# Performance work log

Measured on AMD Instinct MI355X. Metric: run time of the kernel, lower is better.

## Reference

```python
import jax, jax.numpy as jnp
import numpy as np

B, L, D_MODEL, D_FF, H = 2, 2048, 512, 512, 8
DK = D_FF // H


def _lin(key, fan_in, fan_out):
    k1, k2 = jax.random.split(key)
    lim = 1.0 / np.sqrt(fan_in)
    W = jax.random.uniform(k1, (fan_in, fan_out), jnp.float32, -lim, lim)
    b = jax.random.uniform(k2, (fan_out,), jnp.float32, -lim, lim)
    return W, b


def setup_inputs() -> dict:
    key = jax.random.key(0)
    ks = jax.random.split(key, 13)
    x = jax.random.normal(ks[0], (B, L, D_MODEL), jnp.float32)
    x_knowledge = jax.random.normal(ks[1], (B, L, D_MODEL), jnp.float32)
    Wv, bv = _lin(ks[2], D_MODEL, D_FF)
    Wk, bk = _lin(ks[3], D_MODEL, D_FF)
    Wq, bq = _lin(ks[4], D_MODEL, D_FF)
    Wkf, bkf = _lin(ks[5], D_MODEL, D_FF)
    Wqf, bqf = _lin(ks[6], D_MODEL, D_FF)
    Wq2, bq2 = _lin(ks[7], D_FF, D_FF)
    Wk2, bk2 = _lin(ks[8], D_FF, D_FF)
    Wkf2, bkf2 = _lin(ks[9], D_FF, D_FF)
    Wqf2, bqf2 = _lin(ks[10], D_FF, D_FF)
    Wo, bo = _lin(ks[11], D_FF, D_MODEL)
    return dict(x=x, x_knowledge=x_knowledge, Wv=Wv, bv=bv, Wk=Wk, bk=bk,
                Wq=Wq, bq=bq, Wkf=Wkf, bkf=bkf, Wqf=Wqf, bqf=bqf,
                Wq2=Wq2, bq2=bq2, Wk2=Wk2, bk2=bk2, Wqf2=Wqf2, bqf2=bqf2,
                Wkf2=Wkf2, bkf2=bkf2, Wo=Wo, bo=bo)


def reference(x, x_knowledge, Wv, bv, Wk, bk, Wq, bq, Wkf, bkf, Wqf, bqf,
              Wq2, bq2, Wk2, bk2, Wqf2, bqf2, Wkf2, bkf2, Wo, bo):
    b, l, _ = x.shape
    # first projections from d_model -> d_ff
    v = x @ Wv + bv
    k = x @ Wk + bk
    q = x @ Wq + bq
    k_fei = x_knowledge @ Wkf + bkf
    q_fei = x_knowledge @ Wqf + bqf
    # second projections + NONSTANDARD head split: raw reshape (B,L,d_ff)->(B,h,L,dk)
    q = (q @ Wq2 + bq2).reshape(b, H, l, DK)
    k = (k @ Wk2 + bk2).reshape(b, H, l, DK)
    q_fei = (q_fei @ Wqf2 + bqf2).reshape(b, H, l, DK)
    k_fei = (k_fei @ Wkf2 + bkf2).reshape(b, H, l, DK)
    scale = 1.0 / np.sqrt(2.0 * DK).astype(np.float32)
    att = jnp.einsum('bhld,bhmd->bhlm', q, k) * scale
    att_fei = jnp.einsum('bhld,bhmd->bhlm', q_fei, k_fei) * scale
    score = jax.nn.softmax(att + att_fei, axis=-1)  # dropout is identity at eval
    v = v.reshape(b, H, l, DK)
    out = jnp.einsum('bhlm,bhmd->bhld', score, v).reshape(b, l, D_FF)
    return out @ Wo + bo
```

## Files before the change

### kernel.cpp

```cpp
#include <hip/hip_runtime.h>
#include <hip/hip_bf16.h>

typedef unsigned short u16;
typedef unsigned int   u32;
typedef __attribute__((ext_vector_type(8))) short bf16x8;
typedef __attribute__((ext_vector_type(4))) float f32x4;

#define SCALE 0.08838834764831845f
#define SCLOG 0.12752040542575836f

__device__ inline u16 f2bf(float f) {
  u32 u = __builtin_bit_cast(u32, f);
  u = (u + 0x7FFFu + ((u >> 16) & 1u)) >> 16;
  return (u16)u;
}
__device__ inline float bf2f(u16 b) {
  u32 u = (u32)b << 16;
  return __builtin_bit_cast(float, u);
}
__device__ __forceinline__ u16 cvbf(float f) {
  return __builtin_bit_cast(u16, __float2bfloat16(f));
}
__device__ __forceinline__ u32 pkbf(float a, float b) {
  return (u32)cvbf(a) | ((u32)cvbf(b) << 16);
}
__device__ __forceinline__ float fexp2(float x) {
#if __has_builtin(__builtin_amdgcn_exp2f)
  return __builtin_amdgcn_exp2f(x);
#else
  float r; asm("v_exp_f32 %0, %1" : "=v"(r) : "v"(x)); return r;
#endif
}

__device__ __forceinline__ void glds16(const u16* g, u16* l) {
  __builtin_amdgcn_global_load_lds(
      (__attribute__((address_space(1))) void*)g,
      (__attribute__((address_space(3))) void*)l, 16, 0, 0);
}

struct CvPtrs { const float* in[6]; u16* out[6]; int nblk[6]; };

__global__ __launch_bounds__(256) void cvtAll(CvPtrs cp) {
  const int y = blockIdx.y;
  if ((int)blockIdx.x >= cp.nblk[y]) return;
  const float* in = cp.in[y];
  u16* out = cp.out[y];
  const int i = (blockIdx.x * 256 + threadIdx.x) * 8;
  float4 f0 = *(const float4*)(in + i);
  float4 f1 = *(const float4*)(in + i + 4);
  alignas(16) u16 t[8] = {f2bf(f0.x), f2bf(f0.y), f2bf(f0.z), f2bf(f0.w),
                          f2bf(f1.x), f2bf(f1.y), f2bf(f1.z), f2bf(f1.w)};
  *(uint4*)(out + i) = *(const uint4*)t;
}

struct WPtrs { const float* w[10]; const float* b[10]; };

__global__ __launch_bounds__(256) void transposeW(WPtrs p, u16* __restrict__ out,
                                                  float* __restrict__ biasP) {
  __shared__ u16 ts[64][65];
  const int z = blockIdx.z;
  const float sc = (z == 5 || z == 7) ? SCLOG : 1.0f;
  const float* in = p.w[z];
  u16* o = out + (size_t)z * 262144;
  const int t = threadIdx.x;
  const int k0 = blockIdx.y * 64, n0 = blockIdx.x * 64;
  if (blockIdx.x == 0 && blockIdx.y == 0 && (z == 0 || z == 9)) {
    biasP[z * 512 + t]       = p.b[z][t];
    biasP[z * 512 + t + 256] = p.b[z][t + 256];
  }
  for (int pp = 0; pp < 16; ++pp) {
    int id = t + 256 * pp; int r = id >> 6, c = id & 63;
    ts[r][c] = f2bf(in[(size_t)(k0 + r) * 512 + n0 + c] * sc);
  }
  __syncthreads();
  for (int pp = 0; pp < 16; ++pp) {
    int id = t + 256 * pp; int r = id >> 6, c = id & 63;
    o[(size_t)(n0 + r) * 512 + k0 + c] = ts[c][r];
  }
}

struct BEPtrs { const float* b1[4]; const float* w2[4]; const float* b2[4]; };

__global__ __launch_bounds__(256) void biasEff(BEPtrs be, float* __restrict__ biasP) {
  __shared__ float red[16][17];
  const int z = blockIdx.x;
  const int n0 = blockIdx.y * 16;
  const float sc = (z == 0 || z == 2) ? SCLOG : 1.0f;
  const int nl = threadIdx.x & 15, jg = threadIdx.x >> 4;
  const float* b1 = be.b1[z];
  const float* w2 = be.w2[z];
  float s = 0.0f;
  #pragma unroll 4
  for (int jj = 0; jj < 32; ++jj) {
    const int j = jg * 32 + jj;
    s += b1[j] * w2[(size_t)j * 512 + n0 + nl];
  }
  red[jg][nl] = s;
  __syncthreads();
  if (threadIdx.x < 16) {
    float t = 0.0f;
    #pragma unroll
    for (int g = 0; g < 16; ++g) t += red[g][threadIdx.x];
    biasP[(1 + z) * 512 + n0 + threadIdx.x] =
        (t + be.b2[z][n0 + threadIdx.x]) * sc;
  }
}

struct GemmBatch {
  const u16* A[4];
  const u16* Ax;
  int xsplit;
  void* out[5];
  int wrow0, zstride;
};

template <typename TOUT, bool NB>
__global__ __launch_bounds__(256, 4) void gemm4(GemmBatch gb,
    const u16* __restrict__ Wt, const float* __restrict__ biasP) {
  const int tx = blockIdx.x, z = blockIdx.z;
  const u16* A = (tx < gb.xsplit) ? gb.A[z] : gb.Ax;
  const int wrow = gb.wrow0 + z * gb.zstride + tx * 128;
  const int m0 = blockIdx.y * 128;
  const u16* B = Wt + (size_t)wrow * 512;
  const float* bias = biasP + wrow;

  const int t = threadIdx.x, wid = t >> 6, lane = t & 63;
  const int lg = lane >> 4, ln = lane & 15;
  const int wr = wid >> 1, wc = wid & 1;

  __shared__ u16 As[128][64];
  __shared__ u16 Bs[128][64];

  const u16* Ag = A + (size_t)m0 * 512;
  const int lrow = lane >> 3, lch = lane & 7;

  f32x4 acc[4][4];
  #pragma unroll
  for (int i = 0; i < 4; ++i)
    #pragma unroll
    for (int j = 0; j < 4; ++j)
      #pragma unroll
      for (int r = 0; r < 4; ++r) acc[i][j][r] = 0.0f;

  for (int kt = 0; kt < 8; ++kt) {
    #pragma unroll
    for (int c = 0; c < 4; ++c) {
      const int row = (wid * 4 + c) * 8 + lrow;
      const size_t go = (size_t)row * 512 + kt * 64 + lch * 8;
      glds16(Ag + go, &As[(wid * 4 + c) * 8][0]);
      glds16(B  + go, &Bs[(wid * 4 + c) * 8][0]);
    }
    __syncthreads();

    #pragma unroll
    for (int ck = 0; ck < 2; ++ck) {
      bf16x8 af[4], bfr[4];
      #pragma unroll
      for (int mi = 0; mi < 4; ++mi)
        af[mi] = *(const bf16x8*)&As[wr * 64 + mi * 16 + ln][ck * 32 + lg * 8];
      #pragma unroll
      for (int ni = 0; ni < 4; ++ni)
        bfr[ni] = *(const bf16x8*)&Bs[wc * 64 + ni * 16 + ln][ck * 32 + lg * 8];
      #pragma unroll
      for (int mi = 0; mi < 4; ++mi)
        #pragma unroll
        for (int ni = 0; ni < 4; ++ni)
          acc[mi][ni] = __builtin_amdgcn_mfma_f32_16x16x32_bf16(
              af[mi], bfr[ni], acc[mi][ni], 0, 0, 0);
    }
    if (kt < 7) __syncthreads();
  }

  TOUT* C = (TOUT*)gb.out[(wrow >> 9) - (gb.wrow0 >> 9)];
  const int nbase = wrow & 511;
  #pragma unroll
  for (int ni = 0; ni < 4; ++ni) {
    const int colw = wc * 64 + ni * 16 + ln;
    const float bv = NB ? 0.0f : bias[colw];
    const int col = nbase + colw;
    #pragma unroll
    for (int mi = 0; mi < 4; ++mi)
      #pragma unroll
      for (int r = 0; r < 4; ++r) {
        const int row = m0 + wr * 64 + mi * 16 + 4 * lg + r;
        const float val = acc[mi][ni][r] + bv;
        if constexpr (sizeof(TOUT) == 4) C[(size_t)row * 512 + col] = val;
        else                             C[(size_t)row * 512 + col] = f2bf(val);
      }
  }
}

__global__ __launch_bounds__(256) void transposeV(const u16* __restrict__ v1,
                                                  u16* __restrict__ vt) {
  __shared__ u16 ts[64][65];
  const size_t base = (size_t)blockIdx.y * 131072;
  const u16* in = v1 + base;
  u16* out = vt + base;
  const int l0 = blockIdx.x * 64;
  const int t = threadIdx.x;
  const int r = t >> 3, c8 = (t & 7) * 8;
  for (int pp = 0; pp < 2; ++pp) {
    int rr = r + pp * 32;
    *(uint4*)&ts[rr][c8] = *(const uint4*)&in[(size_t)(l0 + rr) * 64 + c8];
  }
  __syncthreads();
  for (int pp = 0; pp < 2; ++pp) {
    int d = r + pp * 32;
    alignas(16) u16 tmp[8];
    #pragma unroll
    for (int i = 0; i < 8; ++i) tmp[i] = ts[c8 + i][d];
    *(uint4*)&out[(size_t)d * 2048 + l0 + c8] = *(const uint4*)tmp;
  }
}

__global__ __launch_bounds__(512) void attn8(
    const u16* __restrict__ q2, const u16* __restrict__ k2,
    const u16* __restrict__ qf2, const u16* __restrict__ kf2,
    const u16* __restrict__ vtg, u16* __restrict__ opart,
    float2* __restrict__ mlbuf) {
  const int id = blockIdx.x;
  const int nid = (id & 7) * 32 + (id >> 3);
  const int split = nid & 1;
  const int qt = (nid >> 1) & 7;
  const int bh = nid >> 4;
  const size_t base = (size_t)bh * 131072;
  const int kv0 = split * 1024;

  const u16* Q  = q2  + base;
  const u16* Qf = qf2 + base;
  u16* Op = opart + (size_t)split * 2097152 + base;

  const int t = threadIdx.x, wid = t >> 6, lane = t & 63;
  const int lg = lane >> 4, ln = lane & 15;
  const int r0 = qt * 256 + wid * 32;

  __shared__ u16 K_s [2][64][64];
  __shared__ u16 Kf_s[2][64][64];
  __shared__ u16 Vt_s[2][64][64];

  const int srow = t >> 3, sch = t & 7;
  const int fsr = (srow & 3) | (((srow >> 3) & 1) << 2);
  const int sw = (sch ^ fsr) * 8;
  const u16* Ksrc  = k2  + base + (size_t)(kv0 + srow) * 64 + sch * 8;
  const u16* Kfsrc = kf2 + base + (size_t)(kv0 + srow) * 64 + sch * 8;
  const u16* Vsrc  = vtg + base + (size_t)srow * 2048 + kv0 + sch * 8;

  bf16x8 aq[2][4];
  #pragma unroll
  for (int qb = 0; qb < 2; ++qb) {
    const int row = r0 + qb * 16 + ln;
    aq[qb][0] = *(const bf16x8*)&Q [row * 64 +      lg * 8];
    aq[qb][1] = *(const bf16x8*)&Q [row * 64 + 32 + lg * 8];
    aq[qb][2] = *(const bf16x8*)&Qf[row * 64 +      lg * 8];
    aq[qb][3] = *(const bf16x8*)&Qf[row * 64 + 32 + lg * 8];
  }

  f32x4 oacc[2][4];
  #pragma unroll
  for (int qb = 0; qb < 2; ++qb)
    #pragma unroll
    for (int df = 0; df < 4; ++df)
      #pragma unroll
      for (int r = 0; r < 4; ++r) oacc[qb][df][r] = 0.0f;
  float m_run[2], l_par[2];
  #pragma unroll
  for (int qb = 0; qb < 2; ++qb) { m_run[qb] = -1e30f; l_par[qb] = 0.0f; }

  const int rbase = 8 * (ln >> 2) + (ln & 3);

  uint4 rk = *(const uint4*)(Ksrc);
  uint4 rf = *(const uint4*)(Kfsrc);
  uint4 rv = *(const uint4*)(Vsrc);
  *(uint4*)&K_s [0][srow][sw] = rk;
  *(uint4*)&Kf_s[0][srow][sw] = rf;
  *(uint4*)&Vt_s[0][srow][sw] = rv;
  __syncthreads();

  int cur = 0;
  for (int kt = 0; kt < 16; ++kt) {
    if (kt < 15) {
      const int ko = (kt + 1) * 4096;
      rk = *(const uint4*)(Ksrc  + ko);
      rf = *(const uint4*)(Kfsrc + ko);
      rv = *(const uint4*)(Vsrc  + (kt + 1) * 64);
    }

    f32x4 s[2][4];
    #pragma unroll
    for (int m = 0; m < 4; ++m) {
      const int rowg = rbase + 4 * (m & 1) + 32 * (m >> 1);
      const int fz = (rowg & 3) | (((rowg >> 3) & 1) << 2);
      bf16x8 a0 = *(const bf16x8*)&K_s [cur][rowg][((0 + lg) ^ fz) * 8];
      bf16x8 a1 = *(const bf16x8*)&K_s [cur][rowg][((4 + lg) ^ fz) * 8];
      bf16x8 a2 = *(const bf16x8*)&Kf_s[cur][rowg][((0 + lg) ^ fz) * 8];
      bf16x8 a3 = *(const bf16x8*)&Kf_s[cur][rowg][((4 + lg) ^ fz) * 8];
      #pragma unroll
      for (int qb = 0; qb < 2; ++qb) {
        f32x4 a;
        #pragma unroll
        for (int r = 0; r < 4; ++r) a[r] = 0.0f;
        a = __builtin_amdgcn_mfma_f32_16x16x32_bf16(a0, aq[qb][0], a, 0, 0, 0);
        a = __builtin_amdgcn_mfma_f32_16x16x32_bf16(a1, aq[qb][1], a, 0, 0, 0);
        a = __builtin_amdgcn_mfma_f32_16x16x32_bf16(a2, aq[qb][2], a, 0, 0, 0);
        a = __builtin_amdgcn_mfma_f32_16x16x32_bf16(a3, aq[qb][3], a, 0, 0, 0);
        s[qb][m] = a;
      }
    }

    float smax[2];
    bool viol = false;
    #pragma unroll
    for (int qb = 0; qb < 2; ++qb) {
      float v = fmaxf(fmaxf(s[qb][0][0], s[qb][0][1]),
                      fmaxf(s[qb][0][2], s[qb][0][3]));
      #pragma unroll
      for (int m = 1; m < 4; ++m)
        v = fmaxf(v, fmaxf(fmaxf(s[qb][m][0], s[qb][m][1]),
                           fmaxf(s[qb][m][2], s[qb][m][3])));
      smax[qb] = v;
      viol = viol || (v > m_run[qb] + 11.0f);
    }
    if (__any(viol)) {
      float corrq[2];
      #pragma unroll
      for (int qb = 0; qb < 2; ++qb) {
        float v = smax[qb];
        v = fmaxf(v, __shfl_xor(v, 16, 64));
        v = fmaxf(v, __shfl_xor(v, 32, 64));
        const float mnew = fmaxf(m_run[qb], v);
        corrq[qb] = fexp2(m_run[qb] - mnew);
        m_run[qb] = mnew;
        l_par[qb] *= corrq[qb];
      }
      #pragma unroll
      for (int qb = 0; qb < 2; ++qb)
        #pragma unroll
        for (int r = 0; r < 4; ++r) {
          const float c = __shfl(corrq[qb], 4 * lg + r, 64);
          #pragma unroll
          for (int df = 0; df < 4; ++df) oacc[qb][df][r] *= c;
        }
    }

    bf16x8 pa[2][2];
    #pragma unroll
    for (int qb = 0; qb < 2; ++qb) {
      float pf[4][4];
      #pragma unroll
      for (int m = 0; m < 4; ++m)
        #pragma unroll
        for (int r = 0; r < 4; ++r) {
          const float p = fexp2(s[qb][m][r] - m_run[qb]);
          l_par[qb] += p;
          pf[m][r] = p;
        }
      #pragma unroll
      for (int kc = 0; kc < 2; ++kc) {
        union { u32 w[4]; bf16x8 v; } U;
        U.w[0] = pkbf(pf[2 * kc][0],     pf[2 * kc][1]);
        U.w[1] = pkbf(pf[2 * kc][2],     pf[2 * kc][3]);
        U.w[2] = pkbf(pf[2 * kc + 1][0], pf[2 * kc + 1][1]);
        U.w[3] = pkbf(pf[2 * kc + 1][2], pf[2 * kc + 1][3]);
        pa[qb][kc] = U.v;
      }
    }

    #pragma unroll
    for (int kc = 0; kc < 2; ++kc)
      #pragma unroll
      for (int df = 0; df < 4; ++df) {
        const int rv = 16 * df + ln;
        const int fz = (rv & 3) | (((rv >> 3) & 1) << 2);
        bf16x8 bv = *(const bf16x8*)&Vt_s[cur][rv][((kc * 4 + lg) ^ fz) * 8];
        oacc[0][df] = __builtin_amdgcn_mfma_f32_16x16x32_bf16(pa[0][kc], bv, oacc[0][df], 0, 0, 0);
        oacc[1][df] = __builtin_amdgcn_mfma_f32_16x16x32_bf16(pa[1][kc], bv, oacc[1][df], 0, 0, 0);
      }

    if (kt < 15) {
      *(uint4*)&K_s [cur ^ 1][srow][sw] = rk;
      *(uint4*)&Kf_s[cur ^ 1][srow][sw] = rf;
      *(uint4*)&Vt_s[cur ^ 1][srow][sw] = rv;
      __syncthreads();
      cur ^= 1;
    }
  }

  #pragma unroll
  for (int qb = 0; qb < 2; ++qb) {
    l_par[qb] += __shfl_xor(l_par[qb], 16, 64);
    l_par[qb] += __shfl_xor(l_par[qb], 32, 64);
  }

  #pragma unroll
  for (int qb = 0; qb < 2; ++qb)
    #pragma unroll
    for (int df = 0; df < 4; ++df)
      #pragma unroll
      for (int r = 0; r < 4; ++r) {
        const int row = r0 + qb * 16 + 4 * lg + r;
        const int col = df * 16 + ln;
        Op[(size_t)row * 64 + col] = f2bf(oacc[qb][df][r]);
      }
  if (lane < 16) {
    #pragma unroll
    for (int qb = 0; qb < 2; ++qb) {
      const int grow = bh * 2048 + r0 + qb * 16 + ln;
      mlbuf[split * 32768 + grow] = make_float2(m_run[qb], l_par[qb]);
    }
  }
}

__global__ __launch_bounds__(256) void combine(
    const u16* __restrict__ opart, const float2* __restrict__ mlbuf,
    u16* __restrict__ att) {
  const int gid = blockIdx.x * 256 + threadIdx.x;
  const int row = gid >> 3, c8 = (gid & 7) * 8;
  const float2 ml1 = mlbuf[row];
  const float2 ml2 = mlbuf[32768 + row];
  const float mx = fmaxf(ml1.x, ml2.x);
  const float a1 = fexp2(ml1.x - mx), a2 = fexp2(ml2.x - mx);
  const float inv = 1.0f / (ml1.y * a1 + ml2.y * a2);
  const float w1 = a1 * inv, w2 = a2 * inv;
  uint4 o1 = *(const uint4*)&opart[(size_t)row * 64 + c8];
  uint4 o2 = *(const uint4*)&opart[2097152 + (size_t)row * 64 + c8];
  const u16* p1 = (const u16*)&o1;
  const u16* p2 = (const u16*)&o2;
  alignas(16) u16 ot[8];
  #pragma unroll
  for (int i = 0; i < 8; ++i)
    ot[i] = cvbf(bf2f(p1[i]) * w1 + bf2f(p2[i]) * w2);
  *(uint4*)&att[(size_t)row * 64 + c8] = *(const uint4*)ot;
}

extern "C" void kernel_launch(void* const* d_in, const int* in_sizes, int n_in,
                              void* d_out, int out_size, void* d_ws, size_t ws_size,
                              hipStream_t stream) {
  const float* x    = (const float*)d_in[0];
  const float* xk   = (const float*)d_in[1];
  const float* Wv   = (const float*)d_in[2];  const float* bv   = (const float*)d_in[3];
  const float* Wk   = (const float*)d_in[4];  const float* bk   = (const float*)d_in[5];
  const float* Wq   = (const float*)d_in[6];  const float* bq   = (const float*)d_in[7];
  const float* Wkf  = (const float*)d_in[8];  const float* bkf  = (const float*)d_in[9];
  const float* Wqf  = (const float*)d_in[10]; const float* bqf  = (const float*)d_in[11];
  const float* Wq2  = (const float*)d_in[12]; const float* bq2  = (const float*)d_in[13];
  const float* Wk2  = (const float*)d_in[14]; const float* bk2  = (const float*)d_in[15];
  const float* Wqf2 = (const float*)d_in[16]; const float* bqf2 = (const float*)d_in[17];
  const float* Wkf2 = (const float*)d_in[18]; const float* bkf2 = (const float*)d_in[19];
  const float* Wo   = (const float*)d_in[20]; const float* bo   = (const float*)d_in[21];

  u16* ws = (u16*)d_ws;
  u16* Wt = ws;
  float* biasP = (float*)(ws + 2621440);
  u16* bufs = ws + 2621440 + 10240;
  const size_t BUF = 2097152;
  u16* b0 = bufs + 0 * BUF;
  u16* b1 = bufs + 1 * BUF;
  u16* b2 = bufs + 2 * BUF;
  u16* b3 = bufs + 3 * BUF;
  u16* b5 = bufs + 5 * BUF;
  u16* b6 = bufs + 6 * BUF;
  u16* b7 = bufs + 7 * BUF;
  u16* b8 = bufs + 8 * BUF;
  float2* mlbuf = (float2*)(bufs + 9 * BUF);
  u16* W1b = bufs + 9 * BUF + 262144;

  CvPtrs cp;
  cp.in[0] = x;   cp.out[0] = b5;             cp.nblk[0] = 1024;
  cp.in[1] = xk;  cp.out[1] = b6;             cp.nblk[1] = 1024;
  cp.in[2] = Wq;  cp.out[2] = W1b;            cp.nblk[2] = 128;
  cp.in[3] = Wk;  cp.out[3] = W1b + 262144;   cp.nblk[3] = 128;
  cp.in[4] = Wqf; cp.out[4] = W1b + 524288;   cp.nblk[4] = 128;
  cp.in[5] = Wkf; cp.out[5] = W1b + 786432;   cp.nblk[5] = 128;
  cvtAll<<<dim3(1024, 6), 256, 0, stream>>>(cp);

  WPtrs wp;
  wp.w[0] = Wv;  wp.w[1] = Wk;  wp.w[2] = Wq;   wp.w[3] = Wkf;  wp.w[4] = Wqf;
  wp.w[5] = Wq2; wp.w[6] = Wk2; wp.w[7] = Wqf2; wp.w[8] = Wkf2; wp.w[9] = Wo;
  wp.b[0] = bv;  wp.b[1] = bk;  wp.b[2] = bq;   wp.b[3] = bkf;  wp.b[4] = bqf;
  wp.b[5] = bq2; wp.b[6] = bk2; wp.b[7] = bqf2; wp.b[8] = bkf2; wp.b[9] = bo;
  transposeW<<<dim3(8, 8, 10), 256, 0, stream>>>(wp, Wt, biasP);

  GemmBatch gw = {};
  gw.A[0] = Wt + 5 * 262144; gw.A[1] = Wt + 6 * 262144;
  gw.A[2] = Wt + 7 * 262144; gw.A[3] = Wt + 8 * 262144;
  gw.Ax = gw.A[0]; gw.xsplit = 100;
  gw.out[0] = Wt + 1 * 262144; gw.out[1] = Wt + 2 * 262144;
  gw.out[2] = Wt + 3 * 262144; gw.out[3] = Wt + 4 * 262144;
  gw.wrow0 = 0; gw.zstride = 512;
  gemm4<u16, true><<<dim3(4, 4, 4), 256, 0, stream>>>(gw, W1b, biasP);

  BEPtrs be;
  be.b1[0] = bq;  be.w2[0] = Wq2;  be.b2[0] = bq2;
  be.b1[1] = bk;  be.w2[1] = Wk2;  be.b2[1] = bk2;
  be.b1[2] = bqf; be.w2[2] = Wqf2; be.b2[2] = bqf2;
  be.b1[3] = bkf; be.w2[3] = Wkf2; be.b2[3] = bkf2;
  biasEff<<<dim3(4, 32), 256, 0, stream>>>(be, biasP);

  GemmBatch g1 = {};
  g1.A[0] = b5;  g1.Ax = b6;  g1.xsplit = 12;
  g1.out[0] = b0; g1.out[1] = b1; g1.out[2] = b3; g1.out[3] = b7; g1.out[4] = b8;
  g1.wrow0 = 0; g1.zstride = 0;
  gemm4<u16, false><<<dim3(20, 32, 1), 256, 0, stream>>>(g1, Wt, biasP);

  transposeV<<<dim3(32, 16), 256, 0, stream>>>(b0, b2);

  attn8<<<dim3(256), 512, 0, stream>>>(b1, b3, b7, b8, b2, b5, mlbuf);

  combine<<<dim3(1024), 256, 0, stream>>>(b5, mlbuf, b0);

  GemmBatch g4 = {};
  g4.A[0] = b0; g4.Ax = b0; g4.xsplit = 100;
  g4.out[0] = d_out;
  g4.wrow0 = 4608; g4.zstride = 0;
  gemm4<float, false><<<dim3(4, 32, 1), 256, 0, stream>>>(g4, Wt, biasP);
}
```

Before: 103.6 us.

## Trim weight transposes, swizzle projection GEMM grid, add MFMA priority hints in attention

transposeW now handles only the six weight matrices whose transposed copies are used, through a constant-memory index map. The first projections for q, k, qf and kf are folded into the second-stage weights, so their transposed copies go unused. The big projection GEMM becomes a 1D-grid kernel with an XCD-aware block remapping, and bf16 conversion uses the hardware intrinsic. In attention, MFMA sections are wrapped in s_setprio and the max and sum reductions are made tree-shaped for more ILP. These aim to cut wasted transpose work and improve cache locality and instruction overlap, but they change several things at once.

```diff
diff --git a/kernel.cpp b/kernel.cpp
--- a/kernel.cpp
+++ b/kernel.cpp
@@ -54,11 +54,12 @@
 }
 
 struct WPtrs { const float* w[10]; const float* b[10]; };
+__constant__ const int ZMAP[6] = {0, 5, 6, 7, 8, 9};
 
 __global__ __launch_bounds__(256) void transposeW(WPtrs p, u16* __restrict__ out,
                                                   float* __restrict__ biasP) {
   __shared__ u16 ts[64][65];
-  const int z = blockIdx.z;
+  const int z = ZMAP[blockIdx.z];
   const float sc = (z == 5 || z == 7) ? SCLOG : 1.0f;
   const float* in = p.w[z];
   u16* o = out + (size_t)z * 262144;
@@ -115,12 +116,12 @@
 };
 
 template <typename TOUT, bool NB>
-__global__ __launch_bounds__(256, 4) void gemm4(GemmBatch gb,
-    const u16* __restrict__ Wt, const float* __restrict__ biasP) {
-  const int tx = blockIdx.x, z = blockIdx.z;
+__device__ __forceinline__ void gemm_body(const GemmBatch& gb,
+    const u16* __restrict__ Wt, const float* __restrict__ biasP,
+    int tx, int my, int z) {
   const u16* A = (tx < gb.xsplit) ? gb.A[z] : gb.Ax;
   const int wrow = gb.wrow0 + z * gb.zstride + tx * 128;
-  const int m0 = blockIdx.y * 128;
+  const int m0 = my * 128;
   const u16* B = Wt + (size_t)wrow * 512;
   const float* bias = biasP + wrow;
 
@@ -185,9 +186,23 @@
         const int row = m0 + wr * 64 + mi * 16 + 4 * lg + r;
         const float val = acc[mi][ni][r] + bv;
         if constexpr (sizeof(TOUT) == 4) C[(size_t)row * 512 + col] = val;
-        else                             C[(size_t)row * 512 + col] = f2bf(val);
-      }
-  }
+        else                             C[(size_t)row * 512 + col] = cvbf(val);
+      }
+  }
+}
+
+template <typename TOUT, bool NB>
+__global__ __launch_bounds__(256, 4) void gemm4(GemmBatch gb,
+    const u16* __restrict__ Wt, const float* __restrict__ biasP) {
+  gemm_body<TOUT, NB>(gb, Wt, biasP, blockIdx.x, blockIdx.y, blockIdx.z);
+}
+
+__global__ __launch_bounds__(256, 4) void gemm5(GemmBatch gb,
+    const u16* __restrict__ Wt, const float* __restrict__ biasP) {
+  const int id = blockIdx.x;
+  const int nid = (id & 7) * 80 + (id >> 3);
+  const int tx = nid % 20, my = nid / 20;
+  gemm_body<u16, false>(gb, Wt, biasP, tx, my, 0);
 }
 
 __global__ __launch_bounds__(256) void transposeV(const u16* __restrict__ v1,
@@ -213,7 +228,7 @@
   }
 }
 
-__global__ __launch_bounds__(512) void attn8(
+__global__ __launch_bounds__(512) void attn9(
     const u16* __restrict__ q2, const u16* __restrict__ k2,
     const u16* __restrict__ qf2, const u16* __restrict__ kf2,
     const u16* __restrict__ vtg, u16* __restrict__ opart,
@@ -286,6 +301,7 @@
     }
 
     f32x4 s[2][4];
+    __builtin_amdgcn_s_setprio(1);
     #pragma unroll
     for (int m = 0; m < 4; ++m) {
       const int rowg = rbase + 4 * (m & 1) + 32 * (m >> 1);
@@ -306,19 +322,19 @@
         s[qb][m] = a;
       }
     }
+    __builtin_amdgcn_s_setprio(0);
 
     float smax[2];
     bool viol = false;
     #pragma unroll
     for (int qb = 0; qb < 2; ++qb) {
-      float v = fmaxf(fmaxf(s[qb][0][0], s[qb][0][1]),
-                      fmaxf(s[qb][0][2], s[qb][0][3]));
-      #pragma unroll
-      for (int m = 1; m < 4; ++m)
-        v = fmaxf(v, fmaxf(fmaxf(s[qb][m][0], s[qb][m][1]),
-                           fmaxf(s[qb][m][2], s[qb][m][3])));
-      smax[qb] = v;
-      viol = viol || (v > m_run[qb] + 11.0f);
+      float vm[4];
+      #pragma unroll
+      for (int m = 0; m < 4; ++m)
+        vm[m] = fmaxf(fmaxf(s[qb][m][0], s[qb][m][1]),
+                      fmaxf(s[qb][m][2], s[qb][m][3]));
+      smax[qb] = fmaxf(fmaxf(vm[0], vm[1]), fmaxf(vm[2], vm[3]));
+      viol = viol || (smax[qb] > m_run[qb] + 11.0f);
     }
     if (__any(viol)) {
       float corrq[2];
@@ -345,15 +361,15 @@
     bf16x8 pa[2][2];
     #pragma unroll
     for (int qb = 0; qb < 2; ++qb) {
-      float pf[4][4];
-      #pragma unroll
-      for (int m = 0; m < 4; ++m)
+      float pf[4][4], ps[4];
+      #pragma unroll
+      for (int m = 0; m < 4; ++m) {
         #pragma unroll
-        for (int r = 0; r < 4; ++r) {
-          const float p = fexp2(s[qb][m][r] - m_run[qb]);
-          l_par[qb] += p;
-          pf[m][r] = p;
-        }
+        for (int r = 0; r < 4; ++r)
+          pf[m][r] = fexp2(s[qb][m][r] - m_run[qb]);
+        ps[m] = (pf[m][0] + pf[m][1]) + (pf[m][2] + pf[m][3]);
+      }
+      l_par[qb] += (ps[0] + ps[1]) + (ps[2] + ps[3]);
       #pragma unroll
       for (int kc = 0; kc < 2; ++kc) {
         union { u32 w[4]; bf16x8 v; } U;
@@ -365,6 +381,7 @@
       }
     }
 
+    __builtin_amdgcn_s_setprio(1);
     #pragma unroll
     for (int kc = 0; kc < 2; ++kc)
       #pragma unroll
@@ -375,6 +392,7 @@
         oacc[0][df] = __builtin_amdgcn_mfma_f32_16x16x32_bf16(pa[0][kc], bv, oacc[0][df], 0, 0, 0);
         oacc[1][df] = __builtin_amdgcn_mfma_f32_16x16x32_bf16(pa[1][kc], bv, oacc[1][df], 0, 0, 0);
       }
+    __builtin_amdgcn_s_setprio(0);
 
     if (kt < 15) {
       *(uint4*)&K_s [cur ^ 1][srow][sw] = rk;
@@ -399,7 +417,7 @@
       for (int r = 0; r < 4; ++r) {
         const int row = r0 + qb * 16 + 4 * lg + r;
         const int col = df * 16 + ln;
-        Op[(size_t)row * 64 + col] = f2bf(oacc[qb][df][r]);
+        Op[(size_t)row * 64 + col] = cvbf(oacc[qb][df][r]);
       }
   if (lane < 16) {
     #pragma unroll
@@ -478,7 +496,7 @@
   wp.w[5] = Wq2; wp.w[6] = Wk2; wp.w[7] = Wqf2; wp.w[8] = Wkf2; wp.w[9] = Wo;
   wp.b[0] = bv;  wp.b[1] = bk;  wp.b[2] = bq;   wp.b[3] = bkf;  wp.b[4] = bqf;
   wp.b[5] = bq2; wp.b[6] = bk2; wp.b[7] = bqf2; wp.b[8] = bkf2; wp.b[9] = bo;
-  transposeW<<<dim3(8, 8, 10), 256, 0, stream>>>(wp, Wt, biasP);
+  transposeW<<<dim3(8, 8, 6), 256, 0, stream>>>(wp, Wt, biasP);
 
   GemmBatch gw = {};
   gw.A[0] = Wt + 5 * 262144; gw.A[1] = Wt + 6 * 262144;
@@ -500,11 +518,11 @@
   g1.A[0] = b5;  g1.Ax = b6;  g1.xsplit = 12;
   g1.out[0] = b0; g1.out[1] = b1; g1.out[2] = b3; g1.out[3] = b7; g1.out[4] = b8;
   g1.wrow0 = 0; g1.zstride = 0;
-  gemm4<u16, false><<<dim3(20, 32, 1), 256, 0, stream>>>(g1, Wt, biasP);
+  gemm5<<<dim3(640), 256, 0, stream>>>(g1, Wt, biasP);
 
   transposeV<<<dim3(32, 16), 256, 0, stream>>>(b0, b2);
 
-  attn8<<<dim3(256), 512, 0, stream>>>(b1, b3, b7, b8, b2, b5, mlbuf);
+  attn9<<<dim3(256), 512, 0, stream>>>(b1, b3, b7, b8, b2, b5, mlbuf);
 
   combine<<<dim3(1024), 256, 0, stream>>>(b5, mlbuf, b0);
 
```

New measurement: 106.0 us. 1.02x slower.
